# Kernel optimization log

Hardware: AMD Instinct MI355X
Metric: run time of the kernel (lower is better)

## Reference

```python
import jax, jax.numpy as jnp
import numpy as np

B, G, N, E, F, H = 16, 8, 512, 8192, 128, 128
BN_EPS = 1e-5


def setup_inputs() -> dict:
    key = jax.random.key(0)
    ks = jax.random.split(key, 6)
    feats = jax.random.normal(ks[0], (B, G, N, F), jnp.float32)
    edges = jax.random.randint(ks[1], (B, G, 2, E), 0, N, dtype=jnp.int32)
    s = lambda k, shape: jax.random.normal(k, shape, jnp.float32) * 0.05
    return {
        "feats": feats,
        "edges": edges,
        "W0": s(ks[2], (F, H)), "b0": jnp.zeros((H,), jnp.float32),
        "W1": s(ks[3], (H, H)), "b1": jnp.zeros((H,), jnp.float32),
        "Wt": s(ks[4], (H, H)), "bt": jnp.zeros((H,), jnp.float32),
        "gamma": jnp.ones((H,), jnp.float32),
        "beta": jnp.zeros((H,), jnp.float32),
        "run_mean": jnp.zeros((H,), jnp.float32),
        "run_var": jnp.ones((H,), jnp.float32),
    }


def _gconv(x, src, dst, W, b):
    # DGL GraphConv with norm='both': relu(D_in^{-1/2} A D_out^{-1/2} X W + b)
    ones = jnp.ones(src.shape, jnp.float32)
    out_deg = jnp.clip(jax.ops.segment_sum(ones, src, num_segments=N), 1.0)
    in_deg = jnp.clip(jax.ops.segment_sum(ones, dst, num_segments=N), 1.0)
    h = x * jax.lax.rsqrt(out_deg)[:, None]          # src normalization
    agg = jax.ops.segment_sum(h[src], dst, num_segments=N)  # SpMM gather+scatter
    h = agg * jax.lax.rsqrt(in_deg)[:, None]          # dst normalization
    return jax.nn.relu(h @ W + b)


def reference(feats, edges, W0, b0, W1, b1, Wt, bt, gamma, beta, run_mean, run_var):
    def per_graph(x, e):
        src, dst = e[0], e[1]
        h = _gconv(x, src, dst, W0, b0)
        h = _gconv(h, src, dst, W1, b1)
        emb = h.mean(axis=0)  # dgl.mean_nodes readout -> [H]
        z = emb @ Wt + bt
        # BatchNorm1d in eval mode (batch of 1 graph embedding)
        z = gamma * (z - run_mean) * jax.lax.rsqrt(run_var + BN_EPS) + beta
        return jax.nn.relu(z)

    xf = feats.reshape(B * G, N, F)
    ef = edges.reshape(B * G, 2, E)
    out = jax.vmap(per_graph)(xf, ef)  # [B*G, H]
    # torch.stack nesting gives (batch, n_graph, 1, H) since mean_nodes returns [1, H]
    return out.reshape(B, G, 1, H)
```

## Files before the change

### kernel.cpp

```cpp
#include <hip/hip_runtime.h>
#include <hip/hip_bf16.h>

#define NN 512
#define NE 8192
#define NG 128
#define FH 128
#define APITCH 68
#define XPITCH 136
#define BN_EPS 1e-5f

typedef __attribute__((ext_vector_type(8))) short s8v;
typedef __attribute__((ext_vector_type(4))) float f4v;
typedef __attribute__((ext_vector_type(4))) unsigned short us4v;
typedef __attribute__((ext_vector_type(4))) unsigned int u4v;

__device__ inline unsigned short f2bf(float x) {
    unsigned u = __float_as_uint(x);
    unsigned r = (u + 0x7fffu + ((u >> 16) & 1u)) >> 16;
    return (unsigned short)r;
}
__device__ inline float bf2f(unsigned short h) { return __uint_as_float(((unsigned)h) << 16); }

__device__ inline unsigned bfpack(int f1bits, int f0bits) {
    return __builtin_amdgcn_perm((unsigned)f1bits, (unsigned)f0bits, 0x07060302u);
}

__global__ __launch_bounds__(1024) void k_build(const int* __restrict__ edges,
                                                float* __restrict__ rs_out,
                                                float* __restrict__ rs_in,
                                                int* __restrict__ bofs,
                                                unsigned short* __restrict__ epk,
                                                const float* __restrict__ W0,
                                                const float* __restrict__ W1,
                                                unsigned short* __restrict__ WP) {
    int g = blockIdx.x;
    int tid = threadIdx.x;

    if (g >= NG) {
        int which = g - NG;
        const float* W = which ? W1 : W0;
        for (int task = tid; task < 2048; task += 1024) {
            int t = task >> 6;
            int lane = task & 63;
            int nt = t >> 2, kk = t & 3;
            int n = nt * 16 + (lane & 15);
            int k0 = kk * 32 + (lane >> 4) * 8;
            unsigned short* dh = WP + ((size_t)which * 2 + 0) * 16384 + ((size_t)t * 64 + lane) * 8;
            unsigned short* dl = WP + ((size_t)which * 2 + 1) * 16384 + ((size_t)t * 64 + lane) * 8;
#pragma unroll
            for (int j = 0; j < 8; j++) {
                float v = W[(size_t)(k0 + j) * FH + n];
                unsigned short h = f2bf(v);
                dh[j] = h;
                dl[j] = f2bf(v - bf2f(h));
            }
        }
        return;
    }

    const int* src = edges + (size_t)g * 2 * NE;
    const int* dst = src + NE;

    __shared__ int degO[NN], degI[NN];
    __shared__ int scanA[1024], scanB[1024];
    __shared__ int fill[1024];
    __shared__ unsigned short pk[NE];

    for (int i = tid; i < NN; i += 1024) { degO[i] = 0; degI[i] = 0; }
    scanA[tid] = 0;
    __syncthreads();

    int rep = tid & 15;
    for (int u = tid; u < NE / 4; u += 1024) {
        int4 s = ((const int4*)src)[u];
        int4 d = ((const int4*)dst)[u];
        atomicAdd(&degO[s.x], 1); atomicAdd(&degO[s.y], 1);
        atomicAdd(&degO[s.z], 1); atomicAdd(&degO[s.w], 1);
        atomicAdd(&degI[d.x], 1); atomicAdd(&degI[d.y], 1);
        atomicAdd(&degI[d.z], 1); atomicAdd(&degI[d.w], 1);
        atomicAdd(&scanA[((((d.x >> 6) << 3) | (s.x >> 6)) << 4) + rep], 1);
        atomicAdd(&scanA[((((d.y >> 6) << 3) | (s.y >> 6)) << 4) + rep], 1);
        atomicAdd(&scanA[((((d.z >> 6) << 3) | (s.z >> 6)) << 4) + rep], 1);
        atomicAdd(&scanA[((((d.w >> 6) << 3) | (s.w >> 6)) << 4) + rep], 1);
    }
    __syncthreads();

    for (int i = tid; i < NN; i += 1024) {
        rs_out[g * NN + i] = rsqrtf((float)max(degO[i], 1));
        rs_in [g * NN + i] = rsqrtf((float)max(degI[i], 1));
    }

    int* sA = scanA; int* sB = scanB;
    for (int off = 1; off < 1024; off <<= 1) {
        int v = sA[tid];
        if (tid >= off) v += sA[tid - off];
        sB[tid] = v;
        __syncthreads();
        int* t = sA; sA = sB; sB = t;
    }
    int excl = tid ? sA[tid - 1] : 0;
    fill[tid] = excl;
    if ((tid & 15) == 0) bofs[g * 65 + (tid >> 4)] = excl;
    if (tid == 0) bofs[g * 65 + 64] = NE;
    __syncthreads();

    for (int u = tid; u < NE / 4; u += 1024) {
        int4 s = ((const int4*)src)[u];
        int4 d = ((const int4*)dst)[u];
        int c, p;
        c = ((((d.x >> 6) << 3) | (s.x >> 6)) << 4) + rep;
        p = atomicAdd(&fill[c], 1); pk[p] = (unsigned short)(((d.x & 63) << 6) | (s.x & 63));
        c = ((((d.y >> 6) << 3) | (s.y >> 6)) << 4) + rep;
        p = atomicAdd(&fill[c], 1); pk[p] = (unsigned short)(((d.y & 63) << 6) | (s.y & 63));
        c = ((((d.z >> 6) << 3) | (s.z >> 6)) << 4) + rep;
        p = atomicAdd(&fill[c], 1); pk[p] = (unsigned short)(((d.z & 63) << 6) | (s.z & 63));
        c = ((((d.w >> 6) << 3) | (s.w >> 6)) << 4) + rep;
        p = atomicAdd(&fill[c], 1); pk[p] = (unsigned short)(((d.w & 63) << 6) | (s.w & 63));
    }
    __syncthreads();
    ((int4*)(epk + (size_t)g * NE))[tid] = ((const int4*)pk)[tid];
}

__global__ __launch_bounds__(256) void k_gemm_f32(const float* __restrict__ X,
                                                  const unsigned short* __restrict__ WPh,
                                                  const unsigned short* __restrict__ WPl,
                                                  const float* __restrict__ rs,
                                                  unsigned short* __restrict__ Yf) {
    __shared__ unsigned short xh[64 * XPITCH];
    __shared__ unsigned short xl[64 * XPITCH];
    int tid = threadIdx.x;
    int sb = blockIdx.y;
    size_t r0 = (size_t)blockIdx.x * NN + (size_t)sb * 64;

    const float4* Xv = (const float4*)(X + r0 * FH);
#pragma unroll
    for (int i = 0; i < 8; i++) {
        int u = tid + i * 256;
        int row = u >> 5, c4 = (u & 31) * 4;
        float4 v = Xv[u];
        int off = row * XPITCH + c4;
        unsigned short h0 = f2bf(v.x), h1 = f2bf(v.y), h2 = f2bf(v.z), h3 = f2bf(v.w);
        us4v hv, lv;
        hv.x = h0; hv.y = h1; hv.z = h2; hv.w = h3;
        lv.x = f2bf(v.x - bf2f(h0));
        lv.y = f2bf(v.y - bf2f(h1));
        lv.z = f2bf(v.z - bf2f(h2));
        lv.w = f2bf(v.w - bf2f(h3));
        *(us4v*)(xh + off) = hv;
        *(us4v*)(xl + off) = lv;
    }
    __syncthreads();

    int lane = tid & 63, w = tid >> 6;
    int quad = lane >> 4, m = lane & 15;
    int arow = w * 16 + m;

    f4v acc[8];
#pragma unroll
    for (int nt = 0; nt < 8; nt++) acc[nt] = (f4v){0.f, 0.f, 0.f, 0.f};

#pragma unroll
    for (int kk = 0; kk < 4; kk++) {
        s8v ah = *(const s8v*)&xh[arow * XPITCH + kk * 32 + quad * 8];
        s8v al = *(const s8v*)&xl[arow * XPITCH + kk * 32 + quad * 8];
#pragma unroll
        for (int nt = 0; nt < 8; nt++) {
            s8v bh = *(const s8v*)(WPh + ((size_t)(nt * 4 + kk) * 64 + lane) * 8);
            s8v bl = *(const s8v*)(WPl + ((size_t)(nt * 4 + kk) * 64 + lane) * 8);
            acc[nt] = __builtin_amdgcn_mfma_f32_16x16x32_bf16(ah, bh, acc[nt], 0, 0, 0);
            acc[nt] = __builtin_amdgcn_mfma_f32_16x16x32_bf16(al, bh, acc[nt], 0, 0, 0);
            acc[nt] = __builtin_amdgcn_mfma_f32_16x16x32_bf16(ah, bl, acc[nt], 0, 0, 0);
        }
    }

    int orow = w * 16 + quad * 4;
    float4 rsv = *(const float4*)(rs + r0 + orow);
    int tag = (w * 2 + (quad >> 1)) & 3;
    int kko = sb * 2 + (w >> 1);
    int j0  = (quad & 1) * 4;
    unsigned short* of = Yf + (size_t)blockIdx.x * (NN * FH);
#pragma unroll
    for (int nt = 0; nt < 8; nt++) {
        us4v v;
        v.x = f2bf(acc[nt][0] * rsv.x);
        v.y = f2bf(acc[nt][1] * rsv.y);
        v.z = f2bf(acc[nt][2] * rsv.z);
        v.w = f2bf(acc[nt][3] * rsv.w);
        *(us4v*)(of + (((size_t)kko * 8 + nt) * 64 + (m + 16 * tag)) * 8 + j0) = v;
    }
}

__global__ __launch_bounds__(512) void k_fused(const unsigned short* __restrict__ Y1f,
                                               const int* __restrict__ bofs,
                                               const unsigned short* __restrict__ epk,
                                               const float* __restrict__ rs_in,
                                               const float* __restrict__ rs_out,
                                               const float* __restrict__ bias,
                                               const unsigned short* __restrict__ WPh,
                                               const unsigned short* __restrict__ WPl,
                                               unsigned short* __restrict__ Y2f) {
    int g  = blockIdx.x;
    int sb = blockIdx.y;
    int tid = threadIdx.x;
    int lane = tid & 63, w8 = tid >> 6;
    int quad = lane >> 4, m = lane & 15;
    int mt = w8 & 3, nh = w8 >> 2;
    int base = sb * 64;

    __shared__ float Af[64 * APITCH];
    __shared__ unsigned short Bs[2 * 8 * 64 * 8];
    unsigned short* hs = (unsigned short*)Af;
    __shared__ float rsin_s[64];
    __shared__ int bo_s[9];

    if (tid < 64) rsin_s[tid] = rs_in[g * NN + base + tid];
    if (tid < 9) bo_s[tid] = bofs[g * 65 + sb * 8 + tid];

    const unsigned short* ep = epk + (size_t)g * NE;
    const int4* Yi4 = (const int4*)(Y1f + (size_t)g * (NN * FH));
    int4* Bi4 = (int4*)Bs;

    f4v acc[4];
#pragma unroll
    for (int j = 0; j < 4; j++) acc[j] = (f4v){0.f, 0.f, 0.f, 0.f};

    for (int p = 0; p < 8; p++) {
        __syncthreads();
        float4 z4 = {0.f, 0.f, 0.f, 0.f};
        for (int i = tid; i < 64 * APITCH / 4; i += 512) ((float4*)Af)[i] = z4;
        __syncthreads();
        for (int e = bo_s[p] + tid; e < bo_s[p + 1]; e += 512) {
            int v = ep[e];
            atomicAdd(&Af[(v >> 6) * APITCH + (v & 63)], 1.0f);
        }
        for (int u = tid; u < 1024; u += 512) Bi4[u] = Yi4[p * 1024 + u];
        __syncthreads();
#pragma unroll
        for (int kkl = 0; kkl < 2; kkl++) {
            s8v bf[4];
#pragma unroll
            for (int j = 0; j < 4; j++)
                bf[j] = *(const s8v*)&Bs[((kkl * 8 + nh * 4 + j) * 64 + lane) * 8];
            const int4* ap = (const int4*)&Af[(mt * 16 + m) * APITCH + kkl * 32 + quad * 8];
            int4 a0 = ap[0];
            int4 a1 = ap[1];
            union { u4v u; s8v s; } cv;
            cv.u.x = bfpack(a0.y, a0.x);
            cv.u.y = bfpack(a0.w, a0.z);
            cv.u.z = bfpack(a1.y, a1.x);
            cv.u.w = bfpack(a1.w, a1.z);
            s8v af = cv.s;
#pragma unroll
            for (int j = 0; j < 4; j++)
                acc[j] = __builtin_amdgcn_mfma_f32_16x16x32_bf16(af, bf[j], acc[j], 0, 0, 0);
        }
    }
    __syncthreads();

#pragma unroll
    for (int j = 0; j < 4; j++) {
        int feat = (nh * 4 + j) * 16 + m;
        float bv = bias[feat];
#pragma unroll
        for (int i = 0; i < 4; i++) {
            int r = mt * 16 + quad * 4 + i;
            float hv = fmaxf(fmaf(rsin_s[r], acc[j][i], bv), 0.f);
            hs[r * XPITCH + feat] = f2bf(hv);
        }
    }
    __syncthreads();

    f4v acc2[4];
#pragma unroll
    for (int j = 0; j < 4; j++) acc2[j] = (f4v){0.f, 0.f, 0.f, 0.f};

#pragma unroll
    for (int kk = 0; kk < 4; kk++) {
        s8v ah = *(const s8v*)&hs[(mt * 16 + m) * XPITCH + kk * 32 + quad * 8];
#pragma unroll
        for (int j = 0; j < 4; j++) {
            int nt = nh * 4 + j;
            s8v bh = *(const s8v*)(WPh + ((size_t)(nt * 4 + kk) * 64 + lane) * 8);
            s8v bl = *(const s8v*)(WPl + ((size_t)(nt * 4 + kk) * 64 + lane) * 8);
            acc2[j] = __builtin_amdgcn_mfma_f32_16x16x32_bf16(ah, bh, acc2[j], 0, 0, 0);
            acc2[j] = __builtin_amdgcn_mfma_f32_16x16x32_bf16(ah, bl, acc2[j], 0, 0, 0);
        }
    }

    int orow = mt * 16 + quad * 4;
    float4 rsv = *(const float4*)(rs_out + (size_t)g * NN + base + orow);
    int tag = (mt * 2 + (quad >> 1)) & 3;
    int kko = sb * 2 + (mt >> 1);
    int j0  = (quad & 1) * 4;
    unsigned short* of = Y2f + (size_t)g * (NN * FH);
#pragma unroll
    for (int j = 0; j < 4; j++) {
        int nt = nh * 4 + j;
        us4v v;
        v.x = f2bf(acc2[j][0] * rsv.x);
        v.y = f2bf(acc2[j][1] * rsv.y);
        v.z = f2bf(acc2[j][2] * rsv.z);
        v.w = f2bf(acc2[j][3] * rsv.w);
        *(us4v*)(of + (((size_t)kko * 8 + nt) * 64 + (m + 16 * tag)) * 8 + j0) = v;
    }
}

__global__ __launch_bounds__(512) void k_gather_mean(const unsigned short* __restrict__ Y2f,
                                                     const int* __restrict__ bofs,
                                                     const unsigned short* __restrict__ epk,
                                                     const float* __restrict__ rs_in,
                                                     const float* __restrict__ bias,
                                                     float* __restrict__ partial) {
    int g  = blockIdx.x;
    int sb = blockIdx.y;
    int tid = threadIdx.x;
    int lane = tid & 63, w8 = tid >> 6;
    int quad = lane >> 4, m = lane & 15;
    int mt = w8 & 3, nh = w8 >> 2;
    int base = sb * 64;

    __shared__ float Af[64 * APITCH];
    __shared__ unsigned short Bs[2 * 8 * 64 * 8];
    float* red = (float*)Af;
    __shared__ float rsin_s[64];
    __shared__ int bo_s[9];

    if (tid < 64) rsin_s[tid] = rs_in[g * NN + base + tid];
    if (tid < 9) bo_s[tid] = bofs[g * 65 + sb * 8 + tid];

    const unsigned short* ep = epk + (size_t)g * NE;
    const int4* Yi4 = (const int4*)(Y2f + (size_t)g * (NN * FH));
    int4* Bi4 = (int4*)Bs;

    f4v acc[4];
#pragma unroll
    for (int j = 0; j < 4; j++) acc[j] = (f4v){0.f, 0.f, 0.f, 0.f};

    for (int p = 0; p < 8; p++) {
        __syncthreads();
        float4 z4 = {0.f, 0.f, 0.f, 0.f};
        for (int i = tid; i < 64 * APITCH / 4; i += 512) ((float4*)Af)[i] = z4;
        __syncthreads();
        for (int e = bo_s[p] + tid; e < bo_s[p + 1]; e += 512) {
            int v = ep[e];
            atomicAdd(&Af[(v >> 6) * APITCH + (v & 63)], 1.0f);
        }
        for (int u = tid; u < 1024; u += 512) Bi4[u] = Yi4[p * 1024 + u];
        __syncthreads();
#pragma unroll
        for (int kkl = 0; kkl < 2; kkl++) {
            s8v bf[4];
#pragma unroll
            for (int j = 0; j < 4; j++)
                bf[j] = *(const s8v*)&Bs[((kkl * 8 + nh * 4 + j) * 64 + lane) * 8];
            const int4* ap = (const int4*)&Af[(mt * 16 + m) * APITCH + kkl * 32 + quad * 8];
            int4 a0 = ap[0];
            int4 a1 = ap[1];
            union { u4v u; s8v s; } cv;
            cv.u.x = bfpack(a0.y, a0.x);
            cv.u.y = bfpack(a0.w, a0.z);
            cv.u.z = bfpack(a1.y, a1.x);
            cv.u.w = bfpack(a1.w, a1.z);
            s8v af = cv.s;
#pragma unroll
            for (int j = 0; j < 4; j++)
                acc[j] = __builtin_amdgcn_mfma_f32_16x16x32_bf16(af, bf[j], acc[j], 0, 0, 0);
        }
    }
    __syncthreads();

#pragma unroll
    for (int j = 0; j < 4; j++) {
        int feat = (nh * 4 + j) * 16 + m;
        float bv = bias[feat];
        float s = 0.f;
#pragma unroll
        for (int i = 0; i < 4; i++) {
            int r = mt * 16 + quad * 4 + i;
            s += fmaxf(fmaf(rsin_s[r], acc[j][i], bv), 0.f);
        }
        red[(w8 * 64 + lane) * 4 + j] = s;
    }
    __syncthreads();
    if (tid < FH) {
        int f = tid;
        int nt = f >> 4, mm = f & 15;
        int nhh = nt >> 2, jj = nt & 3;
        float t = 0.f;
#pragma unroll
        for (int mtt = 0; mtt < 4; mtt++)
#pragma unroll
            for (int q = 0; q < 4; q++)
                t += red[(((nhh * 4 + mtt) * 64) + q * 16 + mm) * 4 + jj];
        partial[((size_t)g * 8 + sb) * FH + f] = t;
    }
}

__global__ __launch_bounds__(128) void k_head(const float* __restrict__ partial,
                                              const float* __restrict__ Wt,
                                              const float* __restrict__ bt,
                                              const float* __restrict__ gamma,
                                              const float* __restrict__ beta,
                                              const float* __restrict__ rmean,
                                              const float* __restrict__ rvar,
                                              float* __restrict__ out) {
    int g = blockIdx.x;
    int j = threadIdx.x;
    __shared__ float e[FH];
    float acc8 = 0.f;
#pragma unroll
    for (int q = 0; q < 8; q++) acc8 += partial[((size_t)g * 8 + q) * FH + j];
    e[j] = acc8 * (1.0f / (float)NN);
    __syncthreads();
    float acc = bt[j];
#pragma unroll 8
    for (int k = 0; k < FH; k++) acc += e[k] * Wt[(size_t)k * FH + j];
    float z = gamma[j] * (acc - rmean[j]) * rsqrtf(rvar[j] + BN_EPS) + beta[j];
    out[g * FH + j] = fmaxf(z, 0.f);
}

extern "C" void kernel_launch(void* const* d_in, const int* in_sizes, int n_in,
                              void* d_out, int out_size, void* d_ws, size_t ws_size,
                              hipStream_t stream) {
    const float* feats = (const float*)d_in[0];
    const int*   edges = (const int*)d_in[1];
    const float* W0    = (const float*)d_in[2];
    const float* b0    = (const float*)d_in[3];
    const float* W1    = (const float*)d_in[4];
    const float* b1    = (const float*)d_in[5];
    const float* Wt    = (const float*)d_in[6];
    const float* bt    = (const float*)d_in[7];
    const float* gamma = (const float*)d_in[8];
    const float* beta  = (const float*)d_in[9];
    const float* rmean = (const float*)d_in[10];
    const float* rvar  = (const float*)d_in[11];
    float* out = (float*)d_out;

    char* w = (char*)d_ws;
    float* rs_out  = (float*)w;   w += sizeof(float) * NG * NN;
    float* rs_in   = (float*)w;   w += sizeof(float) * NG * NN;
    int*   bofs    = (int*)w;     w += sizeof(int) * NG * 65;
    unsigned short* epk = (unsigned short*)w; w += sizeof(unsigned short) * (size_t)NG * NE;
    unsigned short* WP  = (unsigned short*)w; w += sizeof(unsigned short) * 4 * 16384;
    unsigned short* Y1  = (unsigned short*)w; w += sizeof(unsigned short) * (size_t)NG * NN * FH;
    unsigned short* Y2  = (unsigned short*)w; w += sizeof(unsigned short) * (size_t)NG * NN * FH;
    float* partial = (float*)w;   w += sizeof(float) * NG * 8 * FH;

    unsigned short* WPh0 = WP;
    unsigned short* WPl0 = WP + 16384;
    unsigned short* WPh1 = WP + 32768;
    unsigned short* WPl1 = WP + 49152;

    k_build<<<NG + 2, 1024, 0, stream>>>(edges, rs_out, rs_in, bofs, epk, W0, W1, WP);

    k_gemm_f32<<<dim3(NG, 8), 256, 0, stream>>>(feats, WPh0, WPl0, rs_out, Y1);

    k_fused<<<dim3(NG, 8), 512, 0, stream>>>(Y1, bofs, epk, rs_in, rs_out, b0, WPh1, WPl1, Y2);

    k_gather_mean<<<dim3(NG, 8), 512, 0, stream>>>(Y2, bofs, epk, rs_in, b1, partial);

    k_head<<<NG, 128, 0, stream>>>(partial, Wt, bt, gamma, beta, rmean, rvar, out);

    (void)in_sizes; (void)n_in; (void)out_size; (void)ws_size;
}
```

Baseline: 175.2 us.

## Prefetch next panel into registers and fuse head into gather via last-block atomics

In k_fused and k_gather_mean, the next Y panel and the first edge index are loaded into registers during the current iteration's MFMA work, so global latency overlaps with compute and one barrier is dropped. The separate k_head launch is removed. Gather blocks now atomically accumulate partial sums, and the last block per graph (found with a done counter) computes the head. k_build gets an extra block to zero partial and done. This adds register pressure plus atomics and fences, and summation order becomes nondeterministic.

```diff
diff --git a/kernel.cpp b/kernel.cpp
--- a/kernel.cpp
+++ b/kernel.cpp
@@ -32,12 +32,19 @@
                                                 unsigned short* __restrict__ epk,
                                                 const float* __restrict__ W0,
                                                 const float* __restrict__ W1,
-                                                unsigned short* __restrict__ WP) {
+                                                unsigned short* __restrict__ WP,
+                                                float* __restrict__ partial,
+                                                int* __restrict__ done) {
     int g = blockIdx.x;
     int tid = threadIdx.x;
 
     if (g >= NG) {
         int which = g - NG;
+        if (which >= 2) {
+            for (int i = tid; i < NG * FH; i += 1024) partial[i] = 0.f;
+            if (tid < NG) done[tid] = 0;
+            return;
+        }
         const float* W = which ? W1 : W0;
         for (int task = tid; task < 2048; task += 1024) {
             int t = task >> 6;
@@ -213,28 +220,42 @@
     __shared__ float rsin_s[64];
     __shared__ int bo_s[9];
 
-    if (tid < 64) rsin_s[tid] = rs_in[g * NN + base + tid];
-    if (tid < 9) bo_s[tid] = bofs[g * 65 + sb * 8 + tid];
-
     const unsigned short* ep = epk + (size_t)g * NE;
     const int4* Yi4 = (const int4*)(Y1f + (size_t)g * (NN * FH));
     int4* Bi4 = (int4*)Bs;
 
+    int4 rB0 = Yi4[tid];
+    int4 rB1 = Yi4[tid + 512];
+
+    if (tid < 64) rsin_s[tid] = rs_in[g * NN + base + tid];
+    if (tid < 9) bo_s[tid] = bofs[g * 65 + sb * 8 + tid];
+    __syncthreads();
+    int evNext = -1;
+    { int e0 = bo_s[0] + tid; if (e0 < bo_s[1]) evNext = (int)ep[e0]; }
+
     f4v acc[4];
 #pragma unroll
     for (int j = 0; j < 4; j++) acc[j] = (f4v){0.f, 0.f, 0.f, 0.f};
 
     for (int p = 0; p < 8; p++) {
-        __syncthreads();
+        if (p) __syncthreads();
         float4 z4 = {0.f, 0.f, 0.f, 0.f};
         for (int i = tid; i < 64 * APITCH / 4; i += 512) ((float4*)Af)[i] = z4;
+        Bi4[tid] = rB0;
+        Bi4[tid + 512] = rB1;
         __syncthreads();
-        for (int e = bo_s[p] + tid; e < bo_s[p + 1]; e += 512) {
+        if (evNext >= 0) atomicAdd(&Af[(evNext >> 6) * APITCH + (evNext & 63)], 1.0f);
+        for (int e = bo_s[p] + tid + 512; e < bo_s[p + 1]; e += 512) {
             int v = ep[e];
             atomicAdd(&Af[(v >> 6) * APITCH + (v & 63)], 1.0f);
         }
-        for (int u = tid; u < 1024; u += 512) Bi4[u] = Yi4[p * 1024 + u];
         __syncthreads();
+        if (p < 7) {
+            rB0 = Yi4[(p + 1) * 1024 + tid];
+            rB1 = Yi4[(p + 1) * 1024 + tid + 512];
+            int e1 = bo_s[p + 1] + tid;
+            evNext = (e1 < bo_s[p + 2]) ? (int)ep[e1] : -1;
+        }
 #pragma unroll
         for (int kkl = 0; kkl < 2; kkl++) {
             s8v bf[4];
@@ -310,7 +331,15 @@
                                                      const unsigned short* __restrict__ epk,
                                                      const float* __restrict__ rs_in,
                                                      const float* __restrict__ bias,
-                                                     float* __restrict__ partial) {
+                                                     float* __restrict__ partial,
+                                                     int* __restrict__ done,
+                                                     const float* __restrict__ Wt,
+                                                     const float* __restrict__ bt,
+                                                     const float* __restrict__ gamma,
+                                                     const float* __restrict__ beta,
+                                                     const float* __restrict__ rmean,
+                                                     const float* __restrict__ rvar,
+                                                     float* __restrict__ out) {
     int g  = blockIdx.x;
     int sb = blockIdx.y;
     int tid = threadIdx.x;
@@ -324,29 +353,44 @@
     float* red = (float*)Af;
     __shared__ float rsin_s[64];
     __shared__ int bo_s[9];
-
-    if (tid < 64) rsin_s[tid] = rs_in[g * NN + base + tid];
-    if (tid < 9) bo_s[tid] = bofs[g * 65 + sb * 8 + tid];
+    __shared__ int lastFlag;
 
     const unsigned short* ep = epk + (size_t)g * NE;
     const int4* Yi4 = (const int4*)(Y2f + (size_t)g * (NN * FH));
     int4* Bi4 = (int4*)Bs;
 
+    int4 rB0 = Yi4[tid];
+    int4 rB1 = Yi4[tid + 512];
+
+    if (tid < 64) rsin_s[tid] = rs_in[g * NN + base + tid];
+    if (tid < 9) bo_s[tid] = bofs[g * 65 + sb * 8 + tid];
+    __syncthreads();
+    int evNext = -1;
+    { int e0 = bo_s[0] + tid; if (e0 < bo_s[1]) evNext = (int)ep[e0]; }
+
     f4v acc[4];
 #pragma unroll
     for (int j = 0; j < 4; j++) acc[j] = (f4v){0.f, 0.f, 0.f, 0.f};
 
     for (int p = 0; p < 8; p++) {
-        __syncthreads();
+        if (p) __syncthreads();
         float4 z4 = {0.f, 0.f, 0.f, 0.f};
         for (int i = tid; i < 64 * APITCH / 4; i += 512) ((float4*)Af)[i] = z4;
+        Bi4[tid] = rB0;
+        Bi4[tid + 512] = rB1;
         __syncthreads();
-        for (int e = bo_s[p] + tid; e < bo_s[p + 1]; e += 512) {
+        if (evNext >= 0) atomicAdd(&Af[(evNext >> 6) * APITCH + (evNext & 63)], 1.0f);
+        for (int e = bo_s[p] + tid + 512; e < bo_s[p + 1]; e += 512) {
             int v = ep[e];
             atomicAdd(&Af[(v >> 6) * APITCH + (v & 63)], 1.0f);
         }
-        for (int u = tid; u < 1024; u += 512) Bi4[u] = Yi4[p * 1024 + u];
         __syncthreads();
+        if (p < 7) {
+            rB0 = Yi4[(p + 1) * 1024 + tid];
+            rB1 = Yi4[(p + 1) * 1024 + tid + 512];
+            int e1 = bo_s[p + 1] + tid;
+            evNext = (e1 < bo_s[p + 2]) ? (int)ep[e1] : -1;
+        }
 #pragma unroll
         for (int kkl = 0; kkl < 2; kkl++) {
             s8v bf[4];
@@ -392,31 +436,25 @@
 #pragma unroll
             for (int q = 0; q < 4; q++)
                 t += red[(((nhh * 4 + mtt) * 64) + q * 16 + mm) * 4 + jj];
-        partial[((size_t)g * 8 + sb) * FH + f] = t;
-    }
-}
-
-__global__ __launch_bounds__(128) void k_head(const float* __restrict__ partial,
-                                              const float* __restrict__ Wt,
-                                              const float* __restrict__ bt,
-                                              const float* __restrict__ gamma,
-                                              const float* __restrict__ beta,
-                                              const float* __restrict__ rmean,
-                                              const float* __restrict__ rvar,
-                                              float* __restrict__ out) {
-    int g = blockIdx.x;
-    int j = threadIdx.x;
-    __shared__ float e[FH];
-    float acc8 = 0.f;
-#pragma unroll
-    for (int q = 0; q < 8; q++) acc8 += partial[((size_t)g * 8 + q) * FH + j];
-    e[j] = acc8 * (1.0f / (float)NN);
-    __syncthreads();
-    float acc = bt[j];
+        atomicAdd(&partial[(size_t)g * FH + f], t);
+    }
+    __threadfence();
+    __syncthreads();
+    if (tid == 0) lastFlag = (atomicAdd(&done[g], 1) == 7) ? 1 : 0;
+    __syncthreads();
+    if (!lastFlag) return;
+
+    float* eh = (float*)Bs;
+    if (tid < FH) eh[tid] = atomicAdd(&partial[(size_t)g * FH + tid], 0.0f) * (1.0f / (float)NN);
+    __syncthreads();
+    if (tid < FH) {
+        int j = tid;
+        float a2 = bt[j];
 #pragma unroll 8
-    for (int k = 0; k < FH; k++) acc += e[k] * Wt[(size_t)k * FH + j];
-    float z = gamma[j] * (acc - rmean[j]) * rsqrtf(rvar[j] + BN_EPS) + beta[j];
-    out[g * FH + j] = fmaxf(z, 0.f);
+        for (int k = 0; k < FH; k++) a2 += eh[k] * Wt[(size_t)k * FH + j];
+        float z = gamma[j] * (a2 - rmean[j]) * rsqrtf(rvar[j] + BN_EPS) + beta[j];
+        out[g * FH + j] = fmaxf(z, 0.f);
+    }
 }
 
 extern "C" void kernel_launch(void* const* d_in, const int* in_sizes, int n_in,
@@ -444,22 +482,23 @@
     unsigned short* WP  = (unsigned short*)w; w += sizeof(unsigned short) * 4 * 16384;
     unsigned short* Y1  = (unsigned short*)w; w += sizeof(unsigned short) * (size_t)NG * NN * FH;
     unsigned short* Y2  = (unsigned short*)w; w += sizeof(unsigned short) * (size_t)NG * NN * FH;
-    float* partial = (float*)w;   w += sizeof(float) * NG * 8 * FH;
+    float* partial = (float*)w;   w += sizeof(float) * NG * FH;
+    int*   done    = (int*)w;     w += sizeof(int) * NG;
 
     unsigned short* WPh0 = WP;
     unsigned short* WPl0 = WP + 16384;
     unsigned short* WPh1 = WP + 32768;
     unsigned short* WPl1 = WP + 49152;
 
-    k_build<<<NG + 2, 1024, 0, stream>>>(edges, rs_out, rs_in, bofs, epk, W0, W1, WP);
+    k_build<<<NG + 3, 1024, 0, stream>>>(edges, rs_out, rs_in, bofs, epk, W0, W1, WP,
+                                         partial, done);
 
     k_gemm_f32<<<dim3(NG, 8), 256, 0, stream>>>(feats, WPh0, WPl0, rs_out, Y1);
 
     k_fused<<<dim3(NG, 8), 512, 0, stream>>>(Y1, bofs, epk, rs_in, rs_out, b0, WPh1, WPl1, Y2);
 
-    k_gather_mean<<<dim3(NG, 8), 512, 0, stream>>>(Y2, bofs, epk, rs_in, b1, partial);
-
-    k_head<<<NG, 128, 0, stream>>>(partial, Wt, bt, gamma, beta, rmean, rvar, out);
+    k_gather_mean<<<dim3(NG, 8), 512, 0, stream>>>(Y2, bofs, epk, rs_in, b1, partial, done,
+                                                   Wt, bt, gamma, beta, rmean, rvar, out);
 
     (void)in_sizes; (void)n_in; (void)out_size; (void)ws_size;
 }
```

Result: slower. 283.9 us (+62.1%).

## Prefetch next B tile and first edge index into registers during MFMA

Applied to the files above, without the earlier changes.

In both SpMM+GEMM kernels, the next panel of Y features and the first edge index of the next chunk are loaded into registers before the MFMA work of the current chunk runs. They are written to shared memory or applied at the start of the next iteration. The goal is to hide global load latency behind compute. In exchange it uses more registers, which may reduce occupancy, and it changes where barriers fall.

```diff
diff --git a/kernel.cpp b/kernel.cpp
--- a/kernel.cpp
+++ b/kernel.cpp
@@ -213,28 +213,42 @@
     __shared__ float rsin_s[64];
     __shared__ int bo_s[9];
 
-    if (tid < 64) rsin_s[tid] = rs_in[g * NN + base + tid];
-    if (tid < 9) bo_s[tid] = bofs[g * 65 + sb * 8 + tid];
-
     const unsigned short* ep = epk + (size_t)g * NE;
     const int4* Yi4 = (const int4*)(Y1f + (size_t)g * (NN * FH));
     int4* Bi4 = (int4*)Bs;
 
+    int4 rB0 = Yi4[tid];
+    int4 rB1 = Yi4[tid + 512];
+
+    if (tid < 64) rsin_s[tid] = rs_in[g * NN + base + tid];
+    if (tid < 9) bo_s[tid] = bofs[g * 65 + sb * 8 + tid];
+    __syncthreads();
+    int evNext = -1;
+    { int e0 = bo_s[0] + tid; if (e0 < bo_s[1]) evNext = (int)ep[e0]; }
+
     f4v acc[4];
 #pragma unroll
     for (int j = 0; j < 4; j++) acc[j] = (f4v){0.f, 0.f, 0.f, 0.f};
 
     for (int p = 0; p < 8; p++) {
-        __syncthreads();
+        if (p) __syncthreads();
         float4 z4 = {0.f, 0.f, 0.f, 0.f};
         for (int i = tid; i < 64 * APITCH / 4; i += 512) ((float4*)Af)[i] = z4;
+        Bi4[tid] = rB0;
+        Bi4[tid + 512] = rB1;
         __syncthreads();
-        for (int e = bo_s[p] + tid; e < bo_s[p + 1]; e += 512) {
+        if (evNext >= 0) atomicAdd(&Af[(evNext >> 6) * APITCH + (evNext & 63)], 1.0f);
+        for (int e = bo_s[p] + tid + 512; e < bo_s[p + 1]; e += 512) {
             int v = ep[e];
             atomicAdd(&Af[(v >> 6) * APITCH + (v & 63)], 1.0f);
         }
-        for (int u = tid; u < 1024; u += 512) Bi4[u] = Yi4[p * 1024 + u];
         __syncthreads();
+        if (p < 7) {
+            rB0 = Yi4[(p + 1) * 1024 + tid];
+            rB1 = Yi4[(p + 1) * 1024 + tid + 512];
+            int e1 = bo_s[p + 1] + tid;
+            evNext = (e1 < bo_s[p + 2]) ? (int)ep[e1] : -1;
+        }
 #pragma unroll
         for (int kkl = 0; kkl < 2; kkl++) {
             s8v bf[4];
@@ -325,28 +339,42 @@
     __shared__ float rsin_s[64];
     __shared__ int bo_s[9];
 
-    if (tid < 64) rsin_s[tid] = rs_in[g * NN + base + tid];
-    if (tid < 9) bo_s[tid] = bofs[g * 65 + sb * 8 + tid];
-
     const unsigned short* ep = epk + (size_t)g * NE;
     const int4* Yi4 = (const int4*)(Y2f + (size_t)g * (NN * FH));
     int4* Bi4 = (int4*)Bs;
 
+    int4 rB0 = Yi4[tid];
+    int4 rB1 = Yi4[tid + 512];
+
+    if (tid < 64) rsin_s[tid] = rs_in[g * NN + base + tid];
+    if (tid < 9) bo_s[tid] = bofs[g * 65 + sb * 8 + tid];
+    __syncthreads();
+    int evNext = -1;
+    { int e0 = bo_s[0] + tid; if (e0 < bo_s[1]) evNext = (int)ep[e0]; }
+
     f4v acc[4];
 #pragma unroll
     for (int j = 0; j < 4; j++) acc[j] = (f4v){0.f, 0.f, 0.f, 0.f};
 
     for (int p = 0; p < 8; p++) {
-        __syncthreads();
+        if (p) __syncthreads();
         float4 z4 = {0.f, 0.f, 0.f, 0.f};
         for (int i = tid; i < 64 * APITCH / 4; i += 512) ((float4*)Af)[i] = z4;
+        Bi4[tid] = rB0;
+        Bi4[tid + 512] = rB1;
         __syncthreads();
-        for (int e = bo_s[p] + tid; e < bo_s[p + 1]; e += 512) {
+        if (evNext >= 0) atomicAdd(&Af[(evNext >> 6) * APITCH + (evNext & 63)], 1.0f);
+        for (int e = bo_s[p] + tid + 512; e < bo_s[p + 1]; e += 512) {
             int v = ep[e];
             atomicAdd(&Af[(v >> 6) * APITCH + (v & 63)], 1.0f);
         }
-        for (int u = tid; u < 1024; u += 512) Bi4[u] = Yi4[p * 1024 + u];
         __syncthreads();
+        if (p < 7) {
+            rB0 = Yi4[(p + 1) * 1024 + tid];
+            rB1 = Yi4[(p + 1) * 1024 + tid + 512];
+            int e1 = bo_s[p + 1] + tid;
+            evNext = (e1 < bo_s[p + 2]) ? (int)ep[e1] : -1;
+        }
 #pragma unroll
         for (int kkl = 0; kkl < 2; kkl++) {
             s8v bf[4];
```

Measured after the change: 174.0 us. Within noise of the previous version (-0.7%).
